# Kernel tuning notes

Hardware: AMD Instinct MI355X
Metric: run time of the kernel (lower is better)

## Reference

```python
import jax, jax.numpy as jnp
import numpy as np

B, C, H, W = 16, 768, 32, 32
NH, HD, STRIDE = 12, 64, 2
ORF = 2.0  # offset_range_factor
EPS = 1e-5


def dwconv(x, w, b, s):
    # depthwise 3x3 conv, NCHW, weight [C,1,3,3]
    y = jax.lax.conv_general_dilated(
        x, w, window_strides=(s, s), padding=((1, 1), (1, 1)),
        dimension_numbers=('NCHW', 'OIHW', 'NCHW'), feature_group_count=x.shape[1])
    return y + b[None, :, None, None]


def layernorm_c(x, g, b):
    # LayerNorm over channel dim of NCHW (via bhwc as in LayerNormProxy)
    xt = jnp.transpose(x, (0, 2, 3, 1))
    mu = jnp.mean(xt, axis=-1, keepdims=True)
    var = jnp.mean((xt - mu) ** 2, axis=-1, keepdims=True)
    xn = (xt - mu) / jnp.sqrt(var + EPS)
    return jnp.transpose(xn * g + b, (0, 3, 1, 2))


def ref_points(Hh, Ww):
    # matches torch linspace(0.5, H-0.5, H)/H*2-1, stacked as (y, x)
    ry = (jnp.arange(Hh, dtype=jnp.float32) + 0.5) / Hh * 2.0 - 1.0
    rx = (jnp.arange(Ww, dtype=jnp.float32) + 0.5) / Ww * 2.0 - 1.0
    yy, xx = jnp.meshgrid(ry, rx, indexing='ij')
    return jnp.stack([yy, xx], axis=-1)  # [H, W, 2]


def grid_sample_bilinear(inp, grid):
    # inp [B,Cc,Hi,Wi], grid [B,Hg,Wg,2] in (x,y), align_corners=True, zeros padding
    Bb, Cc, Hi, Wi = inp.shape
    gx = (grid[..., 0] + 1.0) * (Wi - 1) * 0.5
    gy = (grid[..., 1] + 1.0) * (Hi - 1) * 0.5
    x0 = jnp.floor(gx); y0 = jnp.floor(gy)
    wx = gx - x0; wy = gy - y0

    def gather(iy, ix):
        valid = (ix >= 0) & (ix <= Wi - 1) & (iy >= 0) & (iy <= Hi - 1)
        iyc = jnp.clip(iy, 0, Hi - 1).astype(jnp.int32)
        ixc = jnp.clip(ix, 0, Wi - 1).astype(jnp.int32)
        vals = jax.vmap(lambda img, a, b: img[:, a, b])(inp, iyc, ixc)  # [B,Cc,Hg,Wg]
        return vals * valid[:, None, :, :].astype(inp.dtype)

    w00 = ((1 - wy) * (1 - wx))[:, None]
    w01 = ((1 - wy) * wx)[:, None]
    w10 = (wy * (1 - wx))[:, None]
    w11 = (wy * wx)[:, None]
    return (gather(y0, x0) * w00 + gather(y0, x0 + 1) * w01
            + gather(y0 + 1, x0) * w10 + gather(y0 + 1, x0 + 1) * w11)


def setup_inputs() -> dict:
    key = jax.random.key(0)
    ks = jax.random.split(key, 16)
    n = lambda k, shp, s: jax.random.normal(k, shp, jnp.float32) * s
    Hk = H // STRIDE
    return {
        'x': n(ks[0], (B, C, H, W), 1.0),
        'wv': n(ks[1], (C, 1, 3, 3), 0.1), 'bv': jnp.zeros((C,), jnp.float32),
        'wq': n(ks[2], (C, 1, 3, 3), 0.1), 'bq': jnp.zeros((C,), jnp.float32),
        'wk': n(ks[3], (C, 1, 3, 3), 0.1), 'bk': jnp.zeros((C,), jnp.float32),
        'w_off1': n(ks[4], (C, 1, 3, 3), 0.1), 'b_off1': jnp.zeros((C,), jnp.float32),
        'ln_g': jnp.ones((C,), jnp.float32), 'ln_b': jnp.zeros((C,), jnp.float32),
        'w_off2': n(ks[5], (2, C, 1, 1), 0.02),
        'rpe_table': n(ks[6], (NH, 2 * Hk - 1, 2 * Hk - 1), 0.01),
        'w_out': n(ks[7], (C, C, 1, 1), 0.02),
    }


def reference(x, wv, bv, wq, bq, wk, bk, w_off1, b_off1, ln_g, ln_b, w_off2, rpe_table, w_out):
    scale = HD ** -0.5
    value = dwconv(x, wv, bv, 1)          # [B,C,H,W]
    query = dwconv(x, wq, bq, 1)          # [B,C,H,W]
    keym = dwconv(x, wk, bk, STRIDE)      # [B,C,Hk,Wk]
    # offset branch: dwconv -> LN -> GELU -> 1x1 conv to 2 channels
    t = jax.nn.gelu(layernorm_c(dwconv(x, w_off1, b_off1, STRIDE), ln_g, ln_b), approximate=False)
    off = jnp.einsum('bchw,pc->bphw', t, w_off2.reshape(2, C))  # [B,2,Hk,Wk] (y,x)
    Hk, Wk = off.shape[2], off.shape[3]
    ns = Hk * Wk
    orange = jnp.array([1.0 / Hk, 1.0 / Wk], jnp.float32).reshape(1, 2, 1, 1)
    off = jnp.tanh(off) * orange * ORF
    off = jnp.transpose(off, (0, 2, 3, 1))  # [B,Hk,Wk,2]
    pos = off + ref_points(Hk, Wk)[None]    # [B,Hk,Wk,2] (y,x); ORF>0 -> no extra tanh

    vs = grid_sample_bilinear(value, pos[..., ::-1]).reshape(B * NH, HD, ns)
    q = query.reshape(B * NH, HD, H * W)
    k = keym.reshape(B * NH, HD, ns)
    attn = jnp.einsum('bcm,bcn->bmn', q, k) * scale  # [B*NH, HW, ns]

    # continuous relative position bias via grid_sample on rpe table
    rpe_bias = jnp.broadcast_to(rpe_table[None], (B, NH, 2 * Hk - 1, 2 * Wk - 1))
    qg = ref_points(H, W).reshape(H * W, 2)
    disp = (qg[None, :, None, :] - pos.reshape(B, ns, 2)[:, None, :, :]) * 0.5  # [B,HW,ns,2]
    bias = grid_sample_bilinear(rpe_bias, disp[..., ::-1]).reshape(B * NH, H * W, ns)

    attn = jax.nn.softmax(attn + bias, axis=-1)
    out = jnp.einsum('bmn,bcn->bcm', attn, vs).reshape(B, C, H, W)
    return jnp.einsum('bchw,oc->bohw', out, w_out.reshape(C, C))
```

## Files before the change

kernel.cpp:

```cpp
#include <hip/hip_runtime.h>
#include <hip/hip_bf16.h>
#include <math.h>

typedef unsigned short u16;
typedef __attribute__((ext_vector_type(8))) short bf8_t;
typedef __attribute__((ext_vector_type(8))) unsigned short us8_t;
typedef __attribute__((ext_vector_type(4))) float f4_t;

#define BB 16
#define CC 768
#define HH 32
#define WW 32
#define HWL 1024
#define NHH 12
#define HDD 64
#define HK 16
#define NS 256
#define RT 31

__device__ inline float us2f(u16 u) {
    return __uint_as_float(((unsigned int)u) << 16);
}
__device__ inline u16 f2us(float f) {
    unsigned int u = __float_as_uint(f);
    unsigned int r = (u + 0x7fffu + ((u >> 16) & 1u)) >> 16;
    return (u16)r;
}

__global__ __launch_bounds__(256) void k_dwconv(
    const float* __restrict__ x,
    const float* __restrict__ wv, const float* __restrict__ bv,
    const float* __restrict__ wq, const float* __restrict__ bq,
    const float* __restrict__ wk, const float* __restrict__ bk,
    const float* __restrict__ wo, const float* __restrict__ bo,
    u16* __restrict__ value, u16* __restrict__ query,
    u16* __restrict__ key, float* __restrict__ tbuf)
{
    __shared__ float xs[34 * 34];
    int blk = blockIdx.x;
    int b = blk / CC, c = blk % CC;
    int tid = threadIdx.x;
    const float* xp = x + (size_t)(b * CC + c) * HWL;

    for (int i = tid; i < 34 * 34; i += 256) {
        int r = i / 34, cc2 = i % 34;
        int gr = r - 1, gc = cc2 - 1;
        float v = 0.f;
        if (gr >= 0 && gr < 32 && gc >= 0 && gc < 32) v = xp[gr * 32 + gc];
        xs[i] = v;
    }
    float wv_[9], wq_[9], wk_[9], wo_[9];
#pragma unroll
    for (int k = 0; k < 9; ++k) {
        wv_[k] = wv[c * 9 + k];
        wq_[k] = wq[c * 9 + k];
        wk_[k] = wk[c * 9 + k];
        wo_[k] = wo[c * 9 + k];
    }
    float bv_ = bv[c], bq_ = bq[c], bk_ = bk[c], bo_ = bo[c];
    __syncthreads();

    {
        int oy = tid >> 3;
        int ox4 = (tid & 7) * 4;
        float xw[3][6];
#pragma unroll
        for (int dy = 0; dy < 3; ++dy)
#pragma unroll
            for (int dx = 0; dx < 6; ++dx)
                xw[dy][dx] = xs[(oy + dy) * 34 + ox4 + dx];
        union { u16 u[4]; ushort4 v; } pv, pq;
#pragma unroll
        for (int j = 0; j < 4; ++j) {
            float av = 0.f, aq = 0.f;
#pragma unroll
            for (int dy = 0; dy < 3; ++dy)
#pragma unroll
                for (int dx = 0; dx < 3; ++dx) {
                    float xv = xw[dy][j + dx];
                    av += xv * wv_[dy * 3 + dx];
                    aq += xv * wq_[dy * 3 + dx];
                }
            pv.u[j] = f2us(av + bv_);
            pq.u[j] = f2us(aq + bq_);
        }
        size_t o = (size_t)(b * CC + c) * HWL + oy * 32 + ox4;
        *(ushort4*)&value[o] = pv.v;
        *(ushort4*)&query[o] = pq.v;
    }
    {
        int oy = tid >> 4, ox = tid & 15;
        float ak = 0.f, ao2 = 0.f;
#pragma unroll
        for (int dy = 0; dy < 3; ++dy)
#pragma unroll
            for (int dx = 0; dx < 3; ++dx) {
                float xv = xs[(2 * oy + dy) * 34 + 2 * ox + dx];
                ak += xv * wk_[dy * 3 + dx];
                ao2 += xv * wo_[dy * 3 + dx];
            }
        key[(size_t)(b * CC + c) * NS + tid] = f2us(ak + bk_);
        tbuf[(size_t)(b * CC + c) * NS + tid] = ao2 + bo_;
    }
}

__global__ __launch_bounds__(256) void k_offset(
    const float* __restrict__ tbuf,
    const float* __restrict__ lng, const float* __restrict__ lnb,
    const float* __restrict__ woff2, float* __restrict__ pos)
{
    __shared__ float sm[16];
    int blk = blockIdx.x;
    int b = blk >> 8;
    int n = blk & 255;
    int tid = threadIdx.x;
    const float* tp = tbuf + (size_t)b * CC * NS + n;
    float tv0 = tp[(size_t)tid * NS];
    float tv1 = tp[(size_t)(tid + 256) * NS];
    float tv2 = tp[(size_t)(tid + 512) * NS];
    float s = tv0 + tv1 + tv2;
    float sq = tv0 * tv0 + tv1 * tv1 + tv2 * tv2;
    for (int o = 32; o; o >>= 1) { s += __shfl_down(s, o); sq += __shfl_down(sq, o); }
    int w = tid >> 6;
    if ((tid & 63) == 0) { sm[w] = s; sm[4 + w] = sq; }
    __syncthreads();
    float st = sm[0] + sm[1] + sm[2] + sm[3];
    float sqt = sm[4] + sm[5] + sm[6] + sm[7];
    float mean = st * (1.f / 768.f);
    float var = sqt * (1.f / 768.f) - mean * mean;
    float rstd = rsqrtf(fmaxf(var, 0.f) + 1e-5f);

    float oy = 0.f, ox = 0.f;
#pragma unroll
    for (int j = 0; j < 3; ++j) {
        int c = tid + j * 256;
        float tvj = (j == 0) ? tv0 : ((j == 1) ? tv1 : tv2);
        float xn = (tvj - mean) * rstd;
        float y = xn * lng[c] + lnb[c];
        float ge = 0.5f * y * (1.f + erff(y * 0.70710678118654752f));
        oy += ge * woff2[c];
        ox += ge * woff2[CC + c];
    }
    for (int o = 32; o; o >>= 1) { oy += __shfl_down(oy, o); ox += __shfl_down(ox, o); }
    __syncthreads();
    if ((tid & 63) == 0) { sm[w] = oy; sm[8 + w] = ox; }
    __syncthreads();
    if (tid == 0) {
        float oyt = sm[0] + sm[1] + sm[2] + sm[3];
        float oxt = sm[8] + sm[9] + sm[10] + sm[11];
        float offy = tanhf(oyt) * 0.125f;
        float offx = tanhf(oxt) * 0.125f;
        int ky = n >> 4, kx = n & 15;
        pos[blk * 2 + 0] = (ky + 0.5f) * 0.125f - 1.f + offy;
        pos[blk * 2 + 1] = (kx + 0.5f) * 0.125f - 1.f + offx;
    }
}

__global__ __launch_bounds__(256) void k_sample(
    const u16* __restrict__ value, const float* __restrict__ pos,
    u16* __restrict__ vst)
{
    __shared__ float psl[NS * 2];
    int cg = blockIdx.x;
    int b  = blockIdx.y;
    int tid = threadIdx.x;
    for (int i = tid; i < NS * 2; i += 256) psl[i] = pos[b * NS * 2 + i];
    __syncthreads();
    int c = cg * 4 + (tid >> 6);
    int nl = tid & 63;
    const u16* vp = value + (size_t)(b * CC + c) * HWL;
    u16* op = vst + (size_t)(b * CC + c) * NS;
#pragma unroll
    for (int j = 0; j < 4; ++j) {
        int n = j * 64 + nl;
        float py = psl[2 * n], px = psl[2 * n + 1];
        float gx = (px + 1.f) * 15.5f;
        float gy = (py + 1.f) * 15.5f;
        float fx = floorf(gx), fy = floorf(gy);
        float wx = gx - fx, wy = gy - fy;
        int ix0 = (int)fx, iy0 = (int)fy;
        int ix1 = ix0 + 1, iy1 = iy0 + 1;
        float m00 = ((unsigned)ix0 < 32u && (unsigned)iy0 < 32u) ? 1.f : 0.f;
        float m01 = ((unsigned)ix1 < 32u && (unsigned)iy0 < 32u) ? 1.f : 0.f;
        float m10 = ((unsigned)ix0 < 32u && (unsigned)iy1 < 32u) ? 1.f : 0.f;
        float m11 = ((unsigned)ix1 < 32u && (unsigned)iy1 < 32u) ? 1.f : 0.f;
        int cx0 = min(max(ix0, 0), 31), cx1 = min(max(ix1, 0), 31);
        int cy0 = min(max(iy0, 0), 31), cy1 = min(max(iy1, 0), 31);
        float w00 = (1.f - wy) * (1.f - wx) * m00;
        float w01 = (1.f - wy) * wx * m01;
        float w10 = wy * (1.f - wx) * m10;
        float w11 = wy * wx * m11;
        float r = w00 * us2f(vp[cy0 * 32 + cx0]) + w01 * us2f(vp[cy0 * 32 + cx1])
                + w10 * us2f(vp[cy1 * 32 + cx0]) + w11 * us2f(vp[cy1 * 32 + cx1]);
        op[n] = f2us(r);
    }
}

__global__ __launch_bounds__(256) void k_transpose(
    const u16* __restrict__ in, u16* __restrict__ out, int R, int S)
{
    __shared__ u16 tile[64][68];
    int bx = blockIdx.x;
    int by = blockIdx.y;
    int bz = blockIdx.z;
    int t = threadIdx.x;
    int ci = (t & 15) * 4;
    int ri = t >> 4;
    const u16* ip = in + (size_t)bz * R * S;
    u16* op = out + (size_t)bz * R * S;
#pragma unroll
    for (int i = 0; i < 4; ++i) {
        int r = ri + i * 16;
        ushort4 v = *(const ushort4*)(ip + (size_t)(by * 64 + r) * S + bx * 64 + ci);
        *(ushort4*)&tile[r][ci] = v;
    }
    __syncthreads();
#pragma unroll
    for (int i = 0; i < 4; ++i) {
        int s = ri + i * 16;
        ushort4 v;
        v.x = tile[ci + 0][s];
        v.y = tile[ci + 1][s];
        v.z = tile[ci + 2][s];
        v.w = tile[ci + 3][s];
        *(ushort4*)(op + (size_t)(bx * 64 + s) * R + by * 64 + ci) = v;
    }
}

__global__ __launch_bounds__(256) void k_cvtw(
    const float* __restrict__ w, u16* __restrict__ wbf)
{
    int i = (blockIdx.x * 256 + threadIdx.x) * 4;
    float4 v = *(const float4*)(w + i);
    union { u16 u[4]; ushort4 v; } pk;
    pk.u[0] = f2us(v.x); pk.u[1] = f2us(v.y);
    pk.u[2] = f2us(v.z); pk.u[3] = f2us(v.w);
    *(ushort4*)(wbf + i) = pk.v;
}

__global__ __launch_bounds__(256, 4) void k_attn(
    const u16* __restrict__ query, const u16* __restrict__ kt,
    const u16* __restrict__ vst, const float* __restrict__ rpe,
    const float* __restrict__ pos, u16* __restrict__ ao)
{
    __shared__ float2 tabp2[35 * 36];
    __shared__ float2 psl2[NS];
    __shared__ u16 Plds[4][16][72];
    __shared__ u16 KsS[4096];
    __shared__ u16 VsS[4096];

    int L = blockIdx.x;
    int xcd = L & 7;
    int t2 = L >> 3;
    int mt = t2 & 15;
    int bh = xcd + 8 * (t2 >> 4);
    int b = bh / NHH, h = bh % NHH;
    int tid = threadIdx.x;
    int w = tid >> 6;
    int l = tid & 63;
    int li = l & 15, lg4 = l >> 4;

    for (int i = tid; i < 35 * 36; i += 256) {
        int r = i / 36, c = i % 36;
        int rr = r - 2;
        int c0i = c - 2, c1i = c - 1;
        float v0 = ((unsigned)rr < 31u && (unsigned)c0i < 31u)
                       ? rpe[h * RT * RT + rr * RT + c0i] : 0.f;
        float v1 = ((unsigned)rr < 31u && (unsigned)c1i < 31u)
                       ? rpe[h * RT * RT + rr * RT + c1i] : 0.f;
        tabp2[i] = make_float2(v0, v1);
    }
    for (int i = tid; i < NS; i += 256) {
        psl2[i] = make_float2(pos[b * NS * 2 + 2 * i], pos[b * NS * 2 + 2 * i + 1]);
    }

    int c0 = h * 64;

#pragma unroll
    for (int it = 0; it < 2; ++it) {
        int Li = tid + it * 256;
        int row = Li >> 3;
        int colb = (Li & 7) * 16;
        us8_t kv = *(const us8_t*)(kt  + (size_t)(b * NS + row) * CC + c0 + colb / 2);
        us8_t vv = *(const us8_t*)(vst + (size_t)(b * CC + c0 + row) * NS + colb / 2);
        int so = (Li * 16) ^ ((row & 7) << 4);
        *(us8_t*)((char*)KsS + so) = kv;
        *(us8_t*)((char*)VsS + so) = vv;
    }
    __syncthreads();

    int m0 = mt * 64 + w * 16;

    bf8_t qf[2];
#pragma unroll
    for (int ks = 0; ks < 2; ++ks) {
        union { short s[8]; bf8_t v; } u;
#pragma unroll
        for (int j = 0; j < 8; ++j)
            u.s[j] = (short)query[(size_t)(b * CC + c0 + ks * 32 + lg4 * 8 + j) * HWL + m0 + li];
        qf[ks] = u.v;
    }
    bf8_t ones;
    {
        union { short s[8]; bf8_t v; } u;
#pragma unroll
        for (int j = 0; j < 8; ++j) u.s[j] = (short)0x3F80;
        ones = u.v;
    }

    f4_t O[4];
#pragma unroll
    for (int ci = 0; ci < 4; ++ci) O[ci] = (f4_t){0.f, 0.f, 0.f, 0.f};
    float mrun[4], lrun[4];
#pragma unroll
    for (int r = 0; r < 4; ++r) { mrun[r] = -1e30f; lrun[r] = 0.f; }

    int mrow = m0 + lg4 * 4;
    float qgy  = ((mrow >> 5) + 0.5f) * 0.0625f - 1.f;
    float qgx0 = ((mrow & 31) + 0.5f) * 0.0625f - 1.f;

    for (int chunk = 0; chunk < 4; ++chunk) {
        int n0 = chunk * 64;

        bf8_t kf[4][2];
#pragma unroll
        for (int ni = 0; ni < 4; ++ni)
#pragma unroll
            for (int ks = 0; ks < 2; ++ks) {
                int addr = (ni * 16 + li) * 128 + ks * 64 + lg4 * 16;
                kf[ni][ks] = *(const bf8_t*)((const char*)KsS + (addr ^ ((li & 7) << 4)));
            }

        us8_t nk[2], nv[2];
        if (chunk < 3) {
            int n1 = n0 + 64;
#pragma unroll
            for (int it = 0; it < 2; ++it) {
                int Li = tid + it * 256;
                int row = Li >> 3;
                int colb = (Li & 7) * 16;
                nk[it] = *(const us8_t*)(kt  + (size_t)(b * NS + n1 + row) * CC + c0 + colb / 2);
                nv[it] = *(const us8_t*)(vst + (size_t)(b * CC + c0 + row) * NS + n1 + colb / 2);
            }
        }

        f4_t s[4];
#pragma unroll
        for (int ni = 0; ni < 4; ++ni) {
            f4_t acc = (f4_t){0.f, 0.f, 0.f, 0.f};
            acc = __builtin_amdgcn_mfma_f32_16x16x32_bf16(qf[0], kf[ni][0], acc, 0, 0, 0);
            acc = __builtin_amdgcn_mfma_f32_16x16x32_bf16(qf[1], kf[ni][1], acc, 0, 0, 0);
            s[ni] = acc;
        }

#pragma unroll
        for (int ni = 0; ni < 4; ++ni) {
            int n = n0 + ni * 16 + li;
            float2 p2 = psl2[n];
            float gy = ((qgy - p2.x) * 0.5f + 1.f) * 15.f;
            float fy = floorf(gy);
            float wy = gy - fy;
            int iy = (int)fy;
            float gxb = (qgx0 - p2.y) * 7.5f + 15.f;
            const float2* row0 = &tabp2[(iy + 2) * 36 + 2];
#pragma unroll
            for (int r = 0; r < 4; ++r) {
                float gx = gxb + r * 0.46875f;
                float fx = floorf(gx);
                float wx = gx - fx;
                int ix = (int)fx;
                float2 t0 = row0[ix];
                float2 t1 = row0[ix + 36];
                float bias = (1.f - wy) * ((1.f - wx) * t0.x + wx * t0.y)
                           + wy * ((1.f - wx) * t1.x + wx * t1.y);
                s[ni][r] = s[ni][r] * 0.125f + bias;
            }
        }

#pragma unroll
        for (int r = 0; r < 4; ++r) {
            float v = fmaxf(fmaxf(s[0][r], s[1][r]), fmaxf(s[2][r], s[3][r]));
            v = fmaxf(v, __shfl_xor(v, 1));
            v = fmaxf(v, __shfl_xor(v, 2));
            v = fmaxf(v, __shfl_xor(v, 4));
            v = fmaxf(v, __shfl_xor(v, 8));
            float mnew = fmaxf(mrun[r], v);
            float sc = __expf(mrun[r] - mnew);
            mrun[r] = mnew;
            lrun[r] *= sc;
#pragma unroll
            for (int ni = 0; ni < 4; ++ni)
                s[ni][r] = __expf(s[ni][r] - mnew);
#pragma unroll
            for (int ci = 0; ci < 4; ++ci) O[ci][r] *= sc;
        }
#pragma unroll
        for (int ni = 0; ni < 4; ++ni)
#pragma unroll
            for (int r = 0; r < 4; ++r)
                Plds[w][lg4 * 4 + r][ni * 16 + li] = f2us(s[ni][r]);

        bf8_t pf[2];
#pragma unroll
        for (int ks = 0; ks < 2; ++ks)
            pf[ks] = *(const bf8_t*)&Plds[w][li][ks * 32 + lg4 * 8];

        f4_t ps = (f4_t){0.f, 0.f, 0.f, 0.f};
        ps = __builtin_amdgcn_mfma_f32_16x16x32_bf16(pf[0], ones, ps, 0, 0, 0);
        ps = __builtin_amdgcn_mfma_f32_16x16x32_bf16(pf[1], ones, ps, 0, 0, 0);
#pragma unroll
        for (int r = 0; r < 4; ++r) lrun[r] += ps[r];

        bf8_t vf[4][2];
#pragma unroll
        for (int ci = 0; ci < 4; ++ci)
#pragma unroll
            for (int ks = 0; ks < 2; ++ks) {
                int addr = (ci * 16 + li) * 128 + ks * 64 + lg4 * 16;
                vf[ci][ks] = *(const bf8_t*)((const char*)VsS + (addr ^ ((li & 7) << 4)));
            }
#pragma unroll
        for (int ci = 0; ci < 4; ++ci) {
            O[ci] = __builtin_amdgcn_mfma_f32_16x16x32_bf16(pf[0], vf[ci][0], O[ci], 0, 0, 0);
            O[ci] = __builtin_amdgcn_mfma_f32_16x16x32_bf16(pf[1], vf[ci][1], O[ci], 0, 0, 0);
        }

        if (chunk < 3) {
            __syncthreads();
#pragma unroll
            for (int it = 0; it < 2; ++it) {
                int Li = tid + it * 256;
                int row = Li >> 3;
                int so = (Li * 16) ^ ((row & 7) << 4);
                *(us8_t*)((char*)KsS + so) = nk[it];
                *(us8_t*)((char*)VsS + so) = nv[it];
            }
            __syncthreads();
        }
    }
    float inv[4];
#pragma unroll
    for (int r = 0; r < 4; ++r) inv[r] = 1.f / lrun[r];
#pragma unroll
    for (int ci = 0; ci < 4; ++ci)
#pragma unroll
        for (int r = 0; r < 4; ++r) {
            int m = m0 + lg4 * 4 + r;
            ao[(size_t)(b * HWL + m) * CC + c0 + ci * 16 + li] = f2us(O[ci][r] * inv[r]);
        }
}

__global__ __launch_bounds__(256) void k_proj(
    const u16* __restrict__ ao, const u16* __restrict__ wbf,
    float* __restrict__ out)
{
    int L = blockIdx.x;
    int xcd = L & 7;
    int t = L >> 3;
    int ot = t % 6;
    int gh = t / 6;
    int g = xcd + 8 * gh;
    int mt = g & 7;
    int b = g >> 3;
    int tid = threadIdx.x;
    int w = tid >> 6, l = tid & 63;
    int li = l & 15, lg4 = l >> 4;
    int o0 = ot * 128 + (w >> 1) * 64;
    int m0 = mt * 128 + (w & 1) * 64;

    const u16* ap = ao + (size_t)b * HWL * CC;

    f4_t acc[4][4];
#pragma unroll
    for (int i = 0; i < 4; ++i)
#pragma unroll
        for (int j = 0; j < 4; ++j) acc[i][j] = (f4_t){0.f, 0.f, 0.f, 0.f};

#pragma unroll 2
    for (int kc = 0; kc < CC; kc += 64) {
        bf8_t af[4][2], bfr[4][2];
#pragma unroll
        for (int i = 0; i < 4; ++i)
#pragma unroll
            for (int ks = 0; ks < 2; ++ks) {
                af[i][ks]  = *(const bf8_t*)(wbf + (size_t)(o0 + i * 16 + li) * CC + kc + ks * 32 + lg4 * 8);
                bfr[i][ks] = *(const bf8_t*)(ap  + (size_t)(m0 + i * 16 + li) * CC + kc + ks * 32 + lg4 * 8);
            }
#pragma unroll
        for (int i = 0; i < 4; ++i)
#pragma unroll
            for (int j = 0; j < 4; ++j) {
                acc[i][j] = __builtin_amdgcn_mfma_f32_16x16x32_bf16(af[i][0], bfr[j][0], acc[i][j], 0, 0, 0);
                acc[i][j] = __builtin_amdgcn_mfma_f32_16x16x32_bf16(af[i][1], bfr[j][1], acc[i][j], 0, 0, 0);
            }
    }
#pragma unroll
    for (int i = 0; i < 4; ++i)
#pragma unroll
        for (int r = 0; r < 4; ++r) {
            int o = o0 + i * 16 + lg4 * 4 + r;
            float* op = out + ((size_t)b * CC + o) * HWL + m0;
#pragma unroll
            for (int j = 0; j < 4; ++j)
                op[j * 16 + li] = acc[i][j][r];
        }
}

extern "C" void kernel_launch(void* const* d_in, const int* in_sizes, int n_in,
                              void* d_out, int out_size, void* d_ws, size_t ws_size,
                              hipStream_t stream) {
    const float* x     = (const float*)d_in[0];
    const float* wv    = (const float*)d_in[1];
    const float* bv    = (const float*)d_in[2];
    const float* wq    = (const float*)d_in[3];
    const float* bq    = (const float*)d_in[4];
    const float* wk    = (const float*)d_in[5];
    const float* bk    = (const float*)d_in[6];
    const float* wo1   = (const float*)d_in[7];
    const float* bo1   = (const float*)d_in[8];
    const float* lng   = (const float*)d_in[9];
    const float* lnb   = (const float*)d_in[10];
    const float* woff2 = (const float*)d_in[11];
    const float* rpe   = (const float*)d_in[12];
    const float* wout  = (const float*)d_in[13];
    float* out = (float*)d_out;

    char* ws = (char*)d_ws;
    size_t off = 0;
    auto alloc = [&](size_t nbytes) -> void* {
        void* p = ws + off;
        off += (nbytes + 255) & ~(size_t)255;
        return p;
    };
    u16*   value = (u16*)  alloc((size_t)BB * CC * HWL * 2);
    u16*   query = (u16*)  alloc((size_t)BB * CC * HWL * 2);
    u16*   key   = (u16*)  alloc((size_t)BB * CC * NS * 2);
    float* tbuf  = (float*)alloc((size_t)BB * NS * CC * 4);
    float* pos   = (float*)alloc((size_t)BB * NS * 2 * 4);
    u16*   ao    = (u16*)  alloc((size_t)BB * HWL * CC * 2);
    u16*   wbf   = (u16*)  alloc((size_t)CC * CC * 2);

    u16* kt  = (u16*)tbuf;
    u16* vst = (u16*)((char*)tbuf + (size_t)BB * NS * CC * 2);

    k_dwconv<<<BB * CC, 256, 0, stream>>>(x, wv, bv, wq, bq, wk, bk, wo1, bo1,
                                          value, query, key, tbuf);
    k_offset<<<BB * NS, 256, 0, stream>>>(tbuf, lng, lnb, woff2, pos);
    k_sample<<<dim3(CC / 4, BB), 256, 0, stream>>>(value, pos, vst);
    k_transpose<<<dim3(NS / 64, CC / 64, BB), 256, 0, stream>>>(key, kt, CC, NS);
    k_cvtw<<<CC * CC / 1024, 256, 0, stream>>>(wout, wbf);
    k_attn<<<dim3(16 * 192), 256, 0, stream>>>(query, kt, vst, rpe, pos, ao);
    k_proj<<<dim3(768), 256, 0, stream>>>(ao, wbf, out);
}
```

Before: 194.4 us.

## Shrink output-projection tiles and software-prefetch next K-chunk in registers

The output-projection GEMM now uses 64x128 block tiles, each wave owning 64x32, instead of 128x128 tiles. This doubles the grid to 1536 blocks and halves the accumulators per wave. The K loop now double-buffers its register fragments, loading the next 64-wide chunk before issuing the MFMAs on the current one, so global-load latency overlaps compute. In exchange, the weight fragments are loaded more often because reuse per wave drops, and the prefetch buffers add register pressure.

```diff
diff --git a/kernel.cpp b/kernel.cpp
--- a/kernel.cpp
+++ b/kernel.cpp
@@ -457,42 +457,69 @@
     int L = blockIdx.x;
     int xcd = L & 7;
     int t = L >> 3;
-    int ot = t % 6;
-    int gh = t / 6;
+    int ot = t % 12;
+    int gh = t / 12;
     int g = xcd + 8 * gh;
     int mt = g & 7;
     int b = g >> 3;
     int tid = threadIdx.x;
     int w = tid >> 6, l = tid & 63;
     int li = l & 15, lg4 = l >> 4;
-    int o0 = ot * 128 + (w >> 1) * 64;
-    int m0 = mt * 128 + (w & 1) * 64;
+    int o0 = ot * 64;
+    int m0 = mt * 128 + w * 32;
 
     const u16* ap = ao + (size_t)b * HWL * CC;
 
-    f4_t acc[4][4];
+    f4_t acc[4][2];
 #pragma unroll
     for (int i = 0; i < 4; ++i)
 #pragma unroll
-        for (int j = 0; j < 4; ++j) acc[i][j] = (f4_t){0.f, 0.f, 0.f, 0.f};
-
-#pragma unroll 2
+        for (int j = 0; j < 2; ++j) acc[i][j] = (f4_t){0.f, 0.f, 0.f, 0.f};
+
+    bf8_t af[4][2], bfr[2][2];
+#pragma unroll
+    for (int i = 0; i < 4; ++i)
+#pragma unroll
+        for (int ks = 0; ks < 2; ++ks)
+            af[i][ks] = *(const bf8_t*)(wbf + (size_t)(o0 + i * 16 + li) * CC + ks * 32 + lg4 * 8);
+#pragma unroll
+    for (int j = 0; j < 2; ++j)
+#pragma unroll
+        for (int ks = 0; ks < 2; ++ks)
+            bfr[j][ks] = *(const bf8_t*)(ap + (size_t)(m0 + j * 16 + li) * CC + ks * 32 + lg4 * 8);
+
     for (int kc = 0; kc < CC; kc += 64) {
-        bf8_t af[4][2], bfr[4][2];
+        bf8_t afn[4][2], bfn[2][2];
+        if (kc + 64 < CC) {
+            int kn = kc + 64;
+#pragma unroll
+            for (int i = 0; i < 4; ++i)
+#pragma unroll
+                for (int ks = 0; ks < 2; ++ks)
+                    afn[i][ks] = *(const bf8_t*)(wbf + (size_t)(o0 + i * 16 + li) * CC + kn + ks * 32 + lg4 * 8);
+#pragma unroll
+            for (int j = 0; j < 2; ++j)
+#pragma unroll
+                for (int ks = 0; ks < 2; ++ks)
+                    bfn[j][ks] = *(const bf8_t*)(ap + (size_t)(m0 + j * 16 + li) * CC + kn + ks * 32 + lg4 * 8);
+        }
 #pragma unroll
         for (int i = 0; i < 4; ++i)
 #pragma unroll
-            for (int ks = 0; ks < 2; ++ks) {
-                af[i][ks]  = *(const bf8_t*)(wbf + (size_t)(o0 + i * 16 + li) * CC + kc + ks * 32 + lg4 * 8);
-                bfr[i][ks] = *(const bf8_t*)(ap  + (size_t)(m0 + i * 16 + li) * CC + kc + ks * 32 + lg4 * 8);
-            }
-#pragma unroll
-        for (int i = 0; i < 4; ++i)
-#pragma unroll
-            for (int j = 0; j < 4; ++j) {
+            for (int j = 0; j < 2; ++j) {
                 acc[i][j] = __builtin_amdgcn_mfma_f32_16x16x32_bf16(af[i][0], bfr[j][0], acc[i][j], 0, 0, 0);
                 acc[i][j] = __builtin_amdgcn_mfma_f32_16x16x32_bf16(af[i][1], bfr[j][1], acc[i][j], 0, 0, 0);
             }
+        if (kc + 64 < CC) {
+#pragma unroll
+            for (int i = 0; i < 4; ++i)
+#pragma unroll
+                for (int ks = 0; ks < 2; ++ks) af[i][ks] = afn[i][ks];
+#pragma unroll
+            for (int j = 0; j < 2; ++j)
+#pragma unroll
+                for (int ks = 0; ks < 2; ++ks) bfr[j][ks] = bfn[j][ks];
+        }
     }
 #pragma unroll
     for (int i = 0; i < 4; ++i)
@@ -501,7 +528,7 @@
             int o = o0 + i * 16 + lg4 * 4 + r;
             float* op = out + ((size_t)b * CC + o) * HWL + m0;
 #pragma unroll
-            for (int j = 0; j < 4; ++j)
+            for (int j = 0; j < 2; ++j)
                 op[j * 16 + li] = acc[i][j][r];
         }
 }
@@ -550,5 +577,5 @@
     k_transpose<<<dim3(NS / 64, CC / 64, BB), 256, 0, stream>>>(key, kt, CC, NS);
     k_cvtw<<<CC * CC / 1024, 256, 0, stream>>>(wout, wbf);
     k_attn<<<dim3(16 * 192), 256, 0, stream>>>(query, kt, vst, rpe, pos, ao);
-    k_proj<<<dim3(768), 256, 0, stream>>>(ao, wbf, out);
-}
+    k_proj<<<dim3(1536), 256, 0, stream>>>(ao, wbf, out);
+}
```

After: 221.3 us. 13.8% more time.
